# Optimization experiments

Measured on AMD Instinct MI355X. Metric: run time of the kernel, lower is better.

Reference implementation:

```python
import jax, jax.numpy as jnp
import numpy as np

N_HEADS = 16
N_EMBED = 1024
HEAD_SIZE = 64


def setup_inputs() -> dict:
    key = jax.random.key(0)
    ks = jax.random.split(key, 6)
    B, T, C = 2, 2048, N_EMBED
    x = jax.random.normal(ks[0], (B, T, C), dtype=jnp.float32)
    s = 1.0 / np.sqrt(C)
    Wq = jax.random.normal(ks[1], (N_HEADS, C, HEAD_SIZE), dtype=jnp.float32) * s
    Wk = jax.random.normal(ks[2], (N_HEADS, C, HEAD_SIZE), dtype=jnp.float32) * s
    Wv = jax.random.normal(ks[3], (N_HEADS, C, HEAD_SIZE), dtype=jnp.float32) * s
    Wo = jax.random.normal(ks[4], (C, C), dtype=jnp.float32) * s
    bo = jax.random.normal(ks[5], (C,), dtype=jnp.float32) * 0.01
    return {"x": x, "Wq": Wq, "Wk": Wk, "Wv": Wv, "Wo": Wo, "bo": bo}


def reference(x, Wq, Wk, Wv, Wo, bo):
    B, T, C = x.shape
    # per-head projections: [B, H, T, D]
    q = jnp.einsum('btc,hcd->bhtd', x, Wq)
    k = jnp.einsum('btc,hcd->bhtd', x, Wk)
    v = jnp.einsum('btc,hcd->bhtd', x, Wv)
    # NOTE: original scales by n_embed**0.5 (C), not head_size**0.5
    scores = jnp.einsum('bhtd,bhsd->bhts', q, k) / jnp.sqrt(jnp.float32(C))
    causal = jnp.tril(jnp.ones((T, T), dtype=bool))
    scores = jnp.where(causal, scores, -jnp.inf)
    wei = jax.nn.softmax(scores, axis=-1)
    out = jnp.einsum('bhts,bhsd->bhtd', wei, v)  # [B, H, T, D]
    out = out.transpose(0, 2, 1, 3).reshape(B, T, C)  # concat heads
    return out @ Wo.T + bo
```

## Files before the change

### kernel.cpp

```cpp
#include <hip/hip_runtime.h>


#define Bsz 2
#define Tsz 2048
#define Cdim 1024
#define Hn 16
#define Dh 64

typedef short bf16x8 __attribute__((ext_vector_type(8)));
typedef float f32x4 __attribute__((ext_vector_type(4)));
typedef unsigned short u16;

#define MFMA(a, b, c) __builtin_amdgcn_mfma_f32_16x16x32_bf16(a, b, c, 0, 0, 0)
#define NEGINF (-__builtin_inff())
#define EXP2(x) __builtin_amdgcn_exp2f(x)

#define GLD16(g, l)                                                            \
  __builtin_amdgcn_global_load_lds((const __attribute__((address_space(1))) void*)(g), \
                                   (__attribute__((address_space(3))) void*)(l), 16, 0, 0)

__device__ __forceinline__ u16 f2bf(float f) {
  unsigned u = __builtin_bit_cast(unsigned, f);
  unsigned r = 0x7fffu + ((u >> 16) & 1u);
  return (u16)((u + r) >> 16);
}

__device__ __forceinline__ unsigned cvtpk(float lo, float hi) {
  unsigned r;
  asm("v_cvt_pk_bf16_f32 %0, %1, %2" : "=v"(r) : "v"(lo), "v"(hi));
  return r;
}

__global__ __launch_bounds__(256) void k_cast_x(const float* __restrict__ x,
                                                u16* __restrict__ xb, int n4) {
  int i = blockIdx.x * 256 + threadIdx.x;
  if (i >= n4) return;
  float4 v = reinterpret_cast<const float4*>(x)[i];
  ushort4 o;
  o.x = f2bf(v.x); o.y = f2bf(v.y); o.z = f2bf(v.z); o.w = f2bf(v.w);
  reinterpret_cast<ushort4*>(xb)[i] = o;
}

__global__ __launch_bounds__(256) void k_cast_w(const float* __restrict__ Wq,
                                                const float* __restrict__ Wk,
                                                const float* __restrict__ Wv,
                                                u16* __restrict__ wt) {
  __shared__ u16 tile[64][68];
  const int mh = blockIdx.y;
  const int m = mh >> 4, h = mh & 15;
  const float* src = (m == 0 ? Wq : m == 1 ? Wk : Wv) + (size_t)h * Cdim * Dh;
  const int c0 = blockIdx.x * 64;
  const int tid = threadIdx.x;
  const int cc = tid >> 4, d4 = (tid & 15) * 4;
#pragma unroll
  for (int i = 0; i < 4; ++i) {
    int c = i * 16 + cc;
    float4 v = *(const float4*)(src + (size_t)(c0 + c) * Dh + d4);
    tile[d4 + 0][c] = f2bf(v.x);
    tile[d4 + 1][c] = f2bf(v.y);
    tile[d4 + 2][c] = f2bf(v.z);
    tile[d4 + 3][c] = f2bf(v.w);
  }
  __syncthreads();
  const int c4 = (tid & 15) * 4, dd = tid >> 4;
#pragma unroll
  for (int i = 0; i < 4; ++i) {
    int d = i * 16 + dd;
    ushort4 o;
    o.x = tile[d][c4]; o.y = tile[d][c4 + 1];
    o.z = tile[d][c4 + 2]; o.w = tile[d][c4 + 3];
    *(ushort4*)(wt + (size_t)(mh * 64 + d) * Cdim + c0 + c4) = o;
  }
}

__global__ __launch_bounds__(256) void k_gemm_qkv(const u16* __restrict__ xb,
                                                  const u16* __restrict__ wt,
                                                  u16* __restrict__ qb,
                                                  u16* __restrict__ kb,
                                                  u16* __restrict__ vtb) {
  __shared__ __align__(16) u16 As[2][4096], Bs[2][4096];
  const int tid = threadIdx.x, lane = tid & 63, wid = tid >> 6;
  const int cl = lane & 15, kg = lane >> 4;
  const int row0 = blockIdx.y * 128, col0 = blockIdx.x * 128;
  const int wrow = (wid >> 1) * 64, wcol = (wid & 1) * 64;
  f32x4 acc[4][4] = {};
  const int csrc = ((lane & 3) ^ ((lane >> 3) & 3)) * 8;
  const u16* a_src = xb + (size_t)(row0 + 32 * wid + (lane >> 2)) * Cdim + csrc;
  const u16* b_src = wt + (size_t)(col0 + 32 * wid + (lane >> 2)) * Cdim + csrc;

  auto stage = [&](int buf, int ke) {
    u16* Ad = &As[buf][1024 * wid];
    u16* Bd = &Bs[buf][1024 * wid];
    GLD16(a_src + ke, Ad);
    GLD16(a_src + 16 * Cdim + ke, Ad + 512);
    GLD16(b_src + ke, Bd);
    GLD16(b_src + 16 * Cdim + ke, Bd + 512);
  };

  const int rdswz = (kg ^ ((cl >> 1) & 3)) * 8;

  stage(0, 0);
  __syncthreads();
  int cur = 0;
  for (int kk = 0; kk < 32; ++kk) {
    if (kk < 31) stage(cur ^ 1, (kk + 1) * 32);
    const u16* ar = &As[cur][(wrow + cl) * 32 + rdswz];
    const u16* br = &Bs[cur][(wcol + cl) * 32 + rdswz];
    bf16x8 af[4], bfr[4];
#pragma unroll
    for (int mi = 0; mi < 4; ++mi) af[mi] = *(const bf16x8*)(ar + mi * 512);
#pragma unroll
    for (int ni = 0; ni < 4; ++ni) bfr[ni] = *(const bf16x8*)(br + ni * 512);
#pragma unroll
    for (int mi = 0; mi < 4; ++mi)
#pragma unroll
      for (int ni = 0; ni < 4; ++ni)
        acc[mi][ni] = MFMA(af[mi], bfr[ni], acc[mi][ni]);
    __syncthreads();
    cur ^= 1;
  }
#pragma unroll
  for (int mi = 0; mi < 4; ++mi) {
#pragma unroll
    for (int ni = 0; ni < 4; ++ni) {
      int n = col0 + wcol + ni * 16 + cl;
      int m = n >> 10, h = (n >> 6) & 15, d = n & 63;
#pragma unroll
      for (int j = 0; j < 4; ++j) {
        int r = row0 + wrow + mi * 16 + kg * 4 + j;
        int b = r >> 11, t = r & 2047;
        float av = acc[mi][ni][j];
        if (m == 0) av *= 0.04508422f;
        u16 v = f2bf(av);
        size_t bh = (size_t)(b * Hn + h);
        if (m == 0)
          qb[(bh * Tsz + t) * Dh + d] = v;
        else if (m == 1)
          kb[(bh * Tsz + t) * Dh + d] = v;
        else
          vtb[(bh * Dh + d) * Tsz + t] = v;
      }
    }
  }
}

__global__ __launch_bounds__(256, 2) void k_attn(const u16* __restrict__ qb,
                                                 const u16* __restrict__ kb,
                                                 const u16* __restrict__ vtb,
                                                 u16* __restrict__ ob) {
  __shared__ __align__(16) u16 KV[2][8192];
  __shared__ __align__(16) u16 Plds[4][2][1024];
  const int lane = threadIdx.x & 63, wid = threadIdx.x >> 6;
  const int cl = lane & 15, kg = lane >> 4;
  const int bid = blockIdx.x;
  const int kdec = bid >> 3;
  const int p = (bid & 7) + ((kdec >> 4) << 3);
  const int tp = kdec & 15;
  const int h = p & 15, b = p >> 4;
  const int tA = tp, tB = 31 - tp;
  const int qrA = tA * 64 + wid * 16;
  const int qrB = tB * 64 + wid * 16;
  const size_t bh = (size_t)(b * Hn + h);
  const u16* Qp = qb + bh * Tsz * Dh;
  const u16* Kp = kb + bh * Tsz * Dh;
  const u16* Vp = vtb + bh * Dh * Tsz;

  const u16* pk_src[2];
  const u16* pv_src[2];
#pragma unroll
  for (int c = 0; c < 2; ++c) {
    int lo = c * 4096 + wid * 1024 + lane * 16;
    int r = lo >> 7, cb = lo & 127;
    int cbs = cb ^ ((r & 7) << 4);
    pk_src[c] = Kp + r * Dh + (cbs >> 1);
    pv_src[c] = Vp + (size_t)r * Tsz + (cbs >> 1);
  }

  auto stage = [&](int buf, int kt) {
    GLD16(pk_src[0] + kt * 4096, &KV[buf][(wid * 1024) >> 1]);
    GLD16(pk_src[1] + kt * 4096, &KV[buf][(4096 + wid * 1024) >> 1]);
    GLD16(pv_src[0] + kt * 64, &KV[buf][(8192 + wid * 1024) >> 1]);
    GLD16(pv_src[1] + kt * 64, &KV[buf][(12288 + wid * 1024) >> 1]);
  };

  bf16x8 qaA0 = *(const bf16x8*)(Qp + (size_t)(qrA + cl) * Dh + kg * 8);
  bf16x8 qaA1 = *(const bf16x8*)(Qp + (size_t)(qrA + cl) * Dh + 32 + kg * 8);
  bf16x8 qaB0 = *(const bf16x8*)(Qp + (size_t)(qrB + cl) * Dh + kg * 8);
  bf16x8 qaB1 = *(const bf16x8*)(Qp + (size_t)(qrB + cl) * Dh + 32 + kg * 8);

  f32x4 oA[4] = {}, oB[4] = {};
  float mA = NEGINF, lA = 0.f, mB = NEGINF, lB = 0.f;

  char* pbA = (char*)&Plds[wid][0][0];
  char* pbB = (char*)&Plds[wid][1][0];
  const int rdoff0 = ((cl << 7) + (kg << 4)) ^ ((cl & 7) << 4);
  const int rdoff1 = ((cl << 7) + 64 + (kg << 4)) ^ ((cl & 7) << 4);
  const int rowoff = wid * 16;
  const int swz0 = (kg * 16) ^ ((cl & 7) << 4);
  const int swz1 = (kg * 16 + 64) ^ ((cl & 7) << 4);

  auto sm_pv = [&](f32x4 s[4], float& m, float& l, f32x4 o[4],
                   const bf16x8 vf[8], char* pb, bool mask) {
    if (mask) {
#pragma unroll
      for (int nt = 0; nt < 4; ++nt)
#pragma unroll
        for (int j = 0; j < 4; ++j)
          if (nt * 16 + kg * 4 + j > rowoff + cl) s[nt][j] = NEGINF;
    }
    float tm = fmaxf(fmaxf(fmaxf(s[0][0], s[0][1]), fmaxf(s[0][2], s[0][3])),
                     fmaxf(fmaxf(s[1][0], s[1][1]), fmaxf(s[1][2], s[1][3])));
    tm = fmaxf(tm, fmaxf(fmaxf(fmaxf(s[2][0], s[2][1]), fmaxf(s[2][2], s[2][3])),
                         fmaxf(fmaxf(s[3][0], s[3][1]), fmaxf(s[3][2], s[3][3]))));
    if (!__all(tm <= m + 8.0f)) {
      tm = fmaxf(tm, __shfl_xor(tm, 16));
      tm = fmaxf(tm, __shfl_xor(tm, 32));
      float mnew = fmaxf(m, tm);
      float corr = EXP2(m - mnew);
      m = mnew;
      l *= corr;
      float c0 = __shfl(corr, kg * 4 + 0);
      float c1 = __shfl(corr, kg * 4 + 1);
      float c2 = __shfl(corr, kg * 4 + 2);
      float c3 = __shfl(corr, kg * 4 + 3);
#pragma unroll
      for (int dt = 0; dt < 4; ++dt) {
        o[dt][0] *= c0; o[dt][1] *= c1; o[dt][2] *= c2; o[dt][3] *= c3;
      }
    }
    float rs = 0.f;
#pragma unroll
    for (int nt = 0; nt < 4; ++nt)
#pragma unroll
      for (int j = 0; j < 4; ++j) {
        float pv = EXP2(s[nt][j] - m);
        s[nt][j] = pv;
        rs += pv;
      }
    l += rs;
#pragma unroll
    for (int nt = 0; nt < 4; ++nt) {
      uint2 pk;
      pk.x = cvtpk(s[nt][0], s[nt][1]);
      pk.y = cvtpk(s[nt][2], s[nt][3]);
      int waddr = ((cl << 7) + (nt << 5) + (kg << 3)) ^ ((cl & 7) << 4);
      *(uint2*)(pb + waddr) = pk;
    }
    bf16x8 pa0 = *(const bf16x8*)(pb + rdoff0);
    bf16x8 pa1 = *(const bf16x8*)(pb + rdoff1);
    __builtin_amdgcn_s_setprio(1);
#pragma unroll
    for (int dt = 0; dt < 4; ++dt) {
      o[dt] = MFMA(pa0, vf[dt * 2], o[dt]);
      o[dt] = MFMA(pa1, vf[dt * 2 + 1], o[dt]);
    }
    __builtin_amdgcn_s_setprio(0);
  };

  const int ntot = tB + 1;
  stage(0, 0);
  __syncthreads();
  int cur = 0;
  for (int t = 0; t < ntot; ++t) {
    if (t + 1 < ntot) stage(cur ^ 1, t + 1);
    char* kvb = (char*)&KV[cur][0];
    bf16x8 ka[8];
#pragma unroll
    for (int nt = 0; nt < 4; ++nt) {
      int rbase = (nt * 16 + cl) << 7;
      ka[nt * 2] = *(const bf16x8*)(kvb + rbase + swz0);
      ka[nt * 2 + 1] = *(const bf16x8*)(kvb + rbase + swz1);
    }
    f32x4 sB[4];
    __builtin_amdgcn_s_setprio(1);
#pragma unroll
    for (int nt = 0; nt < 4; ++nt) {
      f32x4 z = {};
      z = MFMA(ka[nt * 2], qaB0, z);
      z = MFMA(ka[nt * 2 + 1], qaB1, z);
      sB[nt] = z;
    }
    __builtin_amdgcn_s_setprio(0);
    f32x4 sA[4];
    const bool actA = (t <= tA);
    if (actA) {
      __builtin_amdgcn_s_setprio(1);
#pragma unroll
      for (int nt = 0; nt < 4; ++nt) {
        f32x4 z = {};
        z = MFMA(ka[nt * 2], qaA0, z);
        z = MFMA(ka[nt * 2 + 1], qaA1, z);
        sA[nt] = z;
      }
      __builtin_amdgcn_s_setprio(0);
    }
    bf16x8 vf[8];
#pragma unroll
    for (int dt = 0; dt < 4; ++dt) {
      int rbase = 8192 + ((dt * 16 + cl) << 7);
      vf[dt * 2] = *(const bf16x8*)(kvb + rbase + swz0);
      vf[dt * 2 + 1] = *(const bf16x8*)(kvb + rbase + swz1);
    }
    if (actA) sm_pv(sA, mA, lA, oA, vf, pbA, t == tA);
    sm_pv(sB, mB, lB, oB, vf, pbB, t == tB);
    __syncthreads();
    cur ^= 1;
  }

  lA += __shfl_xor(lA, 16); lA += __shfl_xor(lA, 32);
  lB += __shfl_xor(lB, 16); lB += __shfl_xor(lB, 32);
  float iA0 = 1.f / __shfl(lA, kg * 4 + 0), iA1 = 1.f / __shfl(lA, kg * 4 + 1);
  float iA2 = 1.f / __shfl(lA, kg * 4 + 2), iA3 = 1.f / __shfl(lA, kg * 4 + 3);
  float iB0 = 1.f / __shfl(lB, kg * 4 + 0), iB1 = 1.f / __shfl(lB, kg * 4 + 1);
  float iB2 = 1.f / __shfl(lB, kg * 4 + 2), iB3 = 1.f / __shfl(lB, kg * 4 + 3);
  float invA[4] = {iA0, iA1, iA2, iA3};
  float invB[4] = {iB0, iB1, iB2, iB3};
#pragma unroll
  for (int dt = 0; dt < 4; ++dt)
#pragma unroll
    for (int j = 0; j < 4; ++j) {
      int ta = qrA + kg * 4 + j;
      int tb = qrB + kg * 4 + j;
      ob[(size_t)(b * Tsz + ta) * Cdim + h * Dh + dt * 16 + cl] = f2bf(oA[dt][j] * invA[j]);
      ob[(size_t)(b * Tsz + tb) * Cdim + h * Dh + dt * 16 + cl] = f2bf(oB[dt][j] * invB[j]);
    }
}

__global__ __launch_bounds__(256) void k_gemm_out(const u16* __restrict__ ob,
                                                  const u16* __restrict__ wob,
                                                  const float* __restrict__ bo,
                                                  float* __restrict__ out) {
  __shared__ __align__(16) u16 As[2][4096], Bs[2][2048];
  const int tid = threadIdx.x, lane = tid & 63, wid = tid >> 6;
  const int cl = lane & 15, kg = lane >> 4;
  const int row0 = blockIdx.y * 128, col0 = blockIdx.x * 64;
  const int wrow = (wid >> 1) * 64, wcol = (wid & 1) * 32;
  f32x4 acc[4][2] = {};
  const int csrc = ((lane & 3) ^ ((lane >> 3) & 3)) * 8;
  const u16* a_src = ob + (size_t)(row0 + 32 * wid + (lane >> 2)) * Cdim + csrc;
  const u16* b_src = wob + (size_t)(col0 + 16 * wid + (lane >> 2)) * Cdim + csrc;

  auto stage = [&](int buf, int ke) {
    u16* Ad = &As[buf][1024 * wid];
    u16* Bd = &Bs[buf][512 * wid];
    GLD16(a_src + ke, Ad);
    GLD16(a_src + 16 * Cdim + ke, Ad + 512);
    GLD16(b_src + ke, Bd);
  };

  const int rdswz = (kg ^ ((cl >> 1) & 3)) * 8;

  stage(0, 0);
  __syncthreads();
  int cur = 0;
  for (int kk = 0; kk < 32; ++kk) {
    if (kk < 31) stage(cur ^ 1, (kk + 1) * 32);
    const u16* ar = &As[cur][(wrow + cl) * 32 + rdswz];
    const u16* br = &Bs[cur][(wcol + cl) * 32 + rdswz];
    bf16x8 af[4], bfr[2];
#pragma unroll
    for (int mi = 0; mi < 4; ++mi) af[mi] = *(const bf16x8*)(ar + mi * 512);
#pragma unroll
    for (int ni = 0; ni < 2; ++ni) bfr[ni] = *(const bf16x8*)(br + ni * 512);
#pragma unroll
    for (int mi = 0; mi < 4; ++mi)
#pragma unroll
      for (int ni = 0; ni < 2; ++ni)
        acc[mi][ni] = MFMA(af[mi], bfr[ni], acc[mi][ni]);
    __syncthreads();
    cur ^= 1;
  }
#pragma unroll
  for (int mi = 0; mi < 4; ++mi) {
#pragma unroll
    for (int ni = 0; ni < 2; ++ni) {
      int n = col0 + wcol + ni * 16 + cl;
      float bias = bo[n];
#pragma unroll
      for (int j = 0; j < 4; ++j) {
        int r = row0 + wrow + mi * 16 + kg * 4 + j;
        out[(size_t)r * Cdim + n] = acc[mi][ni][j] + bias;
      }
    }
  }
}

extern "C" void kernel_launch(void* const* d_in, const int* in_sizes, int n_in,
                              void* d_out, int out_size, void* d_ws, size_t ws_size,
                              hipStream_t stream) {
  (void)in_sizes; (void)n_in; (void)out_size; (void)ws_size;
  const float* x = (const float*)d_in[0];
  const float* Wq = (const float*)d_in[1];
  const float* Wk = (const float*)d_in[2];
  const float* Wv = (const float*)d_in[3];
  const float* Wo = (const float*)d_in[4];
  const float* bo = (const float*)d_in[5];
  float* out = (float*)d_out;
  char* ws = (char*)d_ws;
  u16* xb = (u16*)(ws);
  u16* wt = (u16*)(ws + (8u << 20));
  u16* wob = (u16*)(ws + (14u << 20));
  u16* qb = (u16*)(ws + (16u << 20));
  u16* kb = (u16*)(ws + (24u << 20));
  u16* vtb = (u16*)(ws + (32u << 20));
  u16* ob = (u16*)(ws + (40u << 20));

  k_cast_x<<<4096, 256, 0, stream>>>(x, xb, Bsz * Tsz * Cdim / 4);
  k_cast_x<<<1024, 256, 0, stream>>>(Wo, wob, Cdim * Cdim / 4);
  k_cast_w<<<dim3(16, 48), 256, 0, stream>>>(Wq, Wk, Wv, wt);
  k_gemm_qkv<<<dim3(24, 32), 256, 0, stream>>>(xb, wt, qb, kb, vtb);
  k_attn<<<512, 256, 0, stream>>>(qb, kb, vtb, ob);
  k_gemm_out<<<dim3(16, 32), 256, 0, stream>>>(ob, wob, bo, out);
}
```

Baseline: 122.6 us.

## Triple-buffer LDS staging in QKV and output GEMMs with explicit vmcnt waits

Both projection GEMM kernels move from double-buffered to triple-buffered global-to-LDS staging. They prefetch two tiles ahead and wait on outstanding loads through explicit s_waitcnt vmcnt counts plus raw s_barrier, instead of a full __syncthreads. The aim is to hide more global memory latency behind the MFMA work. It costs 50% more shared memory per block, which may reduce occupancy, and correctness now relies on hand-counted vmcnt values matching the number of loads each stage issues.

```diff
diff --git a/kernel.cpp b/kernel.cpp
--- a/kernel.cpp
+++ b/kernel.cpp
@@ -78,7 +78,7 @@
                                                   u16* __restrict__ qb,
                                                   u16* __restrict__ kb,
                                                   u16* __restrict__ vtb) {
-  __shared__ __align__(16) u16 As[2][4096], Bs[2][4096];
+  __shared__ __align__(16) u16 As[3][4096], Bs[3][4096];
   const int tid = threadIdx.x, lane = tid & 63, wid = tid >> 6;
   const int cl = lane & 15, kg = lane >> 4;
   const int row0 = blockIdx.y * 128, col0 = blockIdx.x * 128;
@@ -100,10 +100,17 @@
   const int rdswz = (kg ^ ((cl >> 1) & 3)) * 8;
 
   stage(0, 0);
-  __syncthreads();
-  int cur = 0;
+  stage(1, 32);
+  stage(2, 64);
   for (int kk = 0; kk < 32; ++kk) {
-    if (kk < 31) stage(cur ^ 1, (kk + 1) * 32);
+    if (kk < 30)
+      asm volatile("s_waitcnt vmcnt(8)" ::: "memory");
+    else if (kk == 30)
+      asm volatile("s_waitcnt vmcnt(4)" ::: "memory");
+    else
+      asm volatile("s_waitcnt vmcnt(0)" ::: "memory");
+    __builtin_amdgcn_s_barrier();
+    const int cur = kk % 3;
     const u16* ar = &As[cur][(wrow + cl) * 32 + rdswz];
     const u16* br = &Bs[cur][(wcol + cl) * 32 + rdswz];
     bf16x8 af[4], bfr[4];
@@ -116,8 +123,8 @@
 #pragma unroll
       for (int ni = 0; ni < 4; ++ni)
         acc[mi][ni] = MFMA(af[mi], bfr[ni], acc[mi][ni]);
-    __syncthreads();
-    cur ^= 1;
+    __builtin_amdgcn_s_barrier();
+    if (kk + 3 < 32) stage(cur, (kk + 3) * 32);
   }
 #pragma unroll
   for (int mi = 0; mi < 4; ++mi) {
@@ -330,7 +337,7 @@
                                                   const u16* __restrict__ wob,
                                                   const float* __restrict__ bo,
                                                   float* __restrict__ out) {
-  __shared__ __align__(16) u16 As[2][4096], Bs[2][2048];
+  __shared__ __align__(16) u16 As[3][4096], Bs[3][2048];
   const int tid = threadIdx.x, lane = tid & 63, wid = tid >> 6;
   const int cl = lane & 15, kg = lane >> 4;
   const int row0 = blockIdx.y * 128, col0 = blockIdx.x * 64;
@@ -351,10 +358,17 @@
   const int rdswz = (kg ^ ((cl >> 1) & 3)) * 8;
 
   stage(0, 0);
-  __syncthreads();
-  int cur = 0;
+  stage(1, 32);
+  stage(2, 64);
   for (int kk = 0; kk < 32; ++kk) {
-    if (kk < 31) stage(cur ^ 1, (kk + 1) * 32);
+    if (kk < 30)
+      asm volatile("s_waitcnt vmcnt(6)" ::: "memory");
+    else if (kk == 30)
+      asm volatile("s_waitcnt vmcnt(3)" ::: "memory");
+    else
+      asm volatile("s_waitcnt vmcnt(0)" ::: "memory");
+    __builtin_amdgcn_s_barrier();
+    const int cur = kk % 3;
     const u16* ar = &As[cur][(wrow + cl) * 32 + rdswz];
     const u16* br = &Bs[cur][(wcol + cl) * 32 + rdswz];
     bf16x8 af[4], bfr[2];
@@ -367,8 +381,8 @@
 #pragma unroll
       for (int ni = 0; ni < 2; ++ni)
         acc[mi][ni] = MFMA(af[mi], bfr[ni], acc[mi][ni]);
-    __syncthreads();
-    cur ^= 1;
+    __builtin_amdgcn_s_barrier();
+    if (kk + 3 < 32) stage(cur, (kk + 3) * 32);
   }
 #pragma unroll
   for (int mi = 0; mi < 4; ++mi) {
```

Result: faster. 116.6 us (-4.9%).
